# Performance work log

Measured on AMD Instinct MI355X. Metric: run time of the kernel, lower is better.

## Reference

```python
import jax, jax.numpy as jnp
import numpy as np

ALPHA = 0.01  # ELU slope from init kwargs


def setup_inputs() -> dict:
    key = jax.random.key(0)
    k1, k2, k3, k4, k5 = jax.random.split(key, 5)
    B, L, D_IN, D_ATT = 8, 2048, 256, 128
    context = jax.random.normal(k1, (B, L, D_IN), dtype=jnp.float32)
    query = jax.random.normal(k2, (B, L, D_IN), dtype=jnp.float32)
    query_mask = jax.random.randint(k3, (B, L), 0, 2, dtype=jnp.int32)
    # Linear(in_size, attention_size, bias=False) weights (stored as [in, out])
    W_in = jax.random.normal(k4, (D_IN, D_ATT), dtype=jnp.float32) * 0.05
    W_mem = jax.random.normal(k5, (D_IN, D_ATT), dtype=jnp.float32) * 0.05
    return {"context": context, "query": query, "W_in": W_in,
            "W_mem": W_mem, "query_mask": query_mask}


def reference(context, query, W_in, W_mem, query_mask):
    # VariationalDropout is identity at inference; Linear -> ELU(alpha=0.01)
    inp = jax.nn.elu(jnp.einsum('bld,df->blf', context, W_in), ALPHA)   # [B, Lc, Datt]
    mem = jax.nn.elu(jnp.einsum('bld,df->blf', query, W_mem), ALPHA)    # [B, Lq, Datt]
    scale = inp.shape[-1] ** 0.5
    logits = jnp.einsum('bcf,bqf->bcq', inp, mem) / scale               # [B, Lc, Lq]
    big = jnp.finfo(logits.dtype).max
    # mask_diag=True: kill diagonal (self) positions
    Lq = logits.shape[-1]
    eye = jnp.eye(Lq, dtype=bool)
    logits = jnp.where(eye[None, :, :], -big, logits)
    # masked_softmax over the query axis using query_mask [B, Lq]
    valid = (query_mask > 0)[:, None, :]                                # [B, 1, Lq]
    logits = jnp.where(valid, logits, -big)
    score = jax.nn.softmax(logits, axis=-1)                             # [B, Lc, Lq]
    return jnp.einsum('bcq,bqd->bcd', score, query)                     # [B, Lc, D_in]
```

## Files before the change

kernel.cpp:

```cpp
#include <hip/hip_runtime.h>
#include <math.h>

typedef short v4s __attribute__((ext_vector_type(4)));
typedef short v8s __attribute__((ext_vector_type(8)));
typedef float v4f __attribute__((ext_vector_type(4)));

#define L2E 1.4426950408889634f
#define INV_SCALE 0.08838834764831845f
#define SCL2 (INV_SCALE * L2E)

static __device__ __forceinline__ short f2bf(float x) {
    union { float f; unsigned u; } c; c.f = x;
    unsigned u = c.u;
    unsigned r = (u + 0x7fffu + ((u >> 16) & 1u)) >> 16;
    return (short)r;
}

typedef __attribute__((address_space(3))) void lds_vt;
typedef __attribute__((address_space(1))) const void gl_vt;
static __device__ __forceinline__ void gload_lds16(const void* g, void* l) {
    __builtin_amdgcn_global_load_lds((gl_vt*)g, (lds_vt*)l, 16, 0, 0);
}

__global__ __launch_bounds__(256) void k_pre(const float* __restrict__ ctx,
                                             const float* __restrict__ qry,
                                             const float* __restrict__ Win,
                                             const float* __restrict__ Wmem,
                                             const int* __restrict__ qmask,
                                             short* __restrict__ Qa,
                                             short* __restrict__ Ka,
                                             short* __restrict__ VaT,
                                             float* __restrict__ maskadd) {
    __shared__ __align__(16) char sbuf[64 * 264 * 2];
    int x = blockIdx.x;
    int tid = threadIdx.x;
    if (x < 1024) {
        short* WtS = (short*)sbuf;
        int msel = x & 255, isel = (x >> 8) & 1, nh = (x >> 9) & 1;
        const float* X = isel ? qry : ctx;
        const float* W = isel ? Wmem : Win;
        short* Y = isel ? Ka : Qa;
#pragma unroll 8
        for (int i = 0; i < 64; ++i) {
            int id = i * 256 + tid;
            int k = id >> 6, fp = id & 63;
            WtS[fp * 264 + k] = f2bf(W[k * 128 + nh * 64 + fp]);
        }
        __syncthreads();

        int w = tid >> 6, lane = tid & 63;
        int ln = lane & 15, qd = lane >> 4;
        int m0 = msel * 64 + w * 16;
        v4f zero = {0.f, 0.f, 0.f, 0.f};
        v4f o[4];
#pragma unroll
        for (int i = 0; i < 4; ++i) o[i] = zero;
#pragma unroll
        for (int kk = 0; kk < 8; ++kk) {
            const float* xp = X + (size_t)(m0 + ln) * 256 + kk * 32 + qd * 8;
            float4 x0 = *(const float4*)xp;
            float4 x1 = *(const float4*)(xp + 4);
            v8s a;
            a[0] = f2bf(x0.x); a[1] = f2bf(x0.y); a[2] = f2bf(x0.z); a[3] = f2bf(x0.w);
            a[4] = f2bf(x1.x); a[5] = f2bf(x1.y); a[6] = f2bf(x1.z); a[7] = f2bf(x1.w);
#pragma unroll
            for (int nt = 0; nt < 4; ++nt) {
                v8s bfr = *(const v8s*)(WtS + (nt * 16 + ln) * 264 + kk * 32 + qd * 8);
                o[nt] = __builtin_amdgcn_mfma_f32_16x16x32_bf16(a, bfr, o[nt], 0, 0, 0);
            }
        }
#pragma unroll
        for (int nt = 0; nt < 4; ++nt) {
#pragma unroll
            for (int r = 0; r < 4; ++r) {
                float v = o[nt][r];
                v = v > 0.f ? v : 0.01f * (__expf(v) - 1.f);
                Y[(size_t)(m0 + qd * 4 + r) * 128 + (nh * 4 + nt) * 16 + ln] = f2bf(v);
            }
        }
    } else {
        float (*tile)[65] = (float(*)[65])sbuf;
        int t = x - 1024;
        int q0 = (t & 31) * 64, d0 = ((t >> 5) & 3) * 64, b = t >> 7;
        int c = tid & 63;
        int r4 = tid >> 6;
#pragma unroll
        for (int i = 0; i < 16; ++i) {
            int r = r4 + i * 4;
            tile[r][c] = qry[(size_t)(b * 2048 + q0 + r) * 256 + d0 + c];
        }
        __syncthreads();
        int g = c >> 3, j = c & 7;
#pragma unroll
        for (int i = 0; i < 16; ++i) {
            int d = r4 + i * 4;
            int cs = ((g ^ (d & 7)) << 3) | j;
            VaT[(size_t)(b * 256 + d0 + d) * 2048 + q0 + cs] = f2bf(tile[c][d]);
        }
        if (d0 == 0 && tid < 64) {
            int qq = b * 2048 + q0 + tid;
            maskadd[qq] = (qmask[qq] > 0) ? 0.f : -__builtin_inff();
        }
    }
}

__global__ __launch_bounds__(256, 2) void k_attn(const short* __restrict__ Qa,
                                                 const short* __restrict__ Ka,
                                                 const short* __restrict__ VaT,
                                                 const float* __restrict__ maskadd,
                                                 float* __restrict__ out) {
    __shared__ __align__(16) short VaS[2][256 * 64];
    __shared__ __align__(16) short PSb[2][32 * 64];

    const int STEPS = 32;
    int blk = blockIdx.x;
    int b = blk & 7;
    int c0 = (blk >> 3) * 32;

    int tid = threadIdx.x;
    int w = tid >> 6, lane = tid & 63, ln = lane & 15, qd = lane >> 4;

    const short* qbase = Qa + (size_t)(b * 2048) * 128;
    const short* kbase = Ka + (size_t)(b * 2048 + w * 16 + ln) * 128 + qd * 8;
    const short* vbase = VaT + (size_t)(b * 256) * 2048;
    const float* mbase = maskadd + b * 2048 + w * 16 + qd * 4;

    v8s qf[2][4];
#pragma unroll
    for (int ct = 0; ct < 2; ++ct) {
        const short* qp = qbase + (size_t)(c0 + ct * 16 + ln) * 128 + qd * 8;
#pragma unroll
        for (int kk = 0; kk < 4; ++kk) qf[ct][kk] = *(const v8s*)(qp + kk * 32);
    }

    v4f zero = {0.f, 0.f, 0.f, 0.f};
    v4f o[2][4];
#pragma unroll
    for (int i = 0; i < 2; ++i)
#pragma unroll
        for (int j = 0; j < 4; ++j) o[i][j] = zero;
    float lacc[2] = {0.f, 0.f};

    auto stageV = [&](int q0s, int buf) {
        short* base = &VaS[buf][0] + w * 4096;
#pragma unroll
        for (int j = 0; j < 8; ++j) {
            int U = (w * 8 + j) * 64 + lane;
            int d = U >> 3, cc = U & 7;
            gload_lds16(vbase + (size_t)d * 2048 + q0s + cc * 8,
                        base + j * 512);
        }
    };

    stageV(0, 0);
    v8s kfA[4], kfB[4];
    float4 mkA, mkB;
#pragma unroll
    for (int kk = 0; kk < 4; ++kk) kfA[kk] = *(const v8s*)(kbase + kk * 32);
    mkA = *(const float4*)(mbase);

#define ATT_STEP(IT, KFC, MKC, KFN, MKN) do {                                  \
    int q0 = (IT) * 64;                                                        \
    int pb = (IT) & 1;                                                         \
    int itn = ((IT) + 1) & (STEPS - 1);                                        \
    stageV(itn * 64, pb ^ 1);                                                  \
    {                                                                          \
        const short* kp = kbase + (size_t)itn * 8192;                          \
        _Pragma("unroll")                                                      \
        for (int kk = 0; kk < 4; ++kk) KFN[kk] = *(const v8s*)(kp + kk * 32);  \
        MKN = *(const float4*)(mbase + itn * 64);                              \
    }                                                                          \
      \
    asm volatile("s_waitcnt vmcnt(13)" ::: "memory");                          \
    short* PScur = &PSb[pb][0];                                                \
    int kvb = q0 + w * 16 + qd * 4;                                            \
    _Pragma("unroll")                                                          \
    for (int ct = 0; ct < 2; ++ct) {                                           \
        v4f s = zero;                                                          \
        _Pragma("unroll")                                                      \
        for (int kk = 0; kk < 4; ++kk)                                         \
            s = __builtin_amdgcn_mfma_f32_16x16x32_bf16(KFC[kk], qf[ct][kk],   \
                                                        s, 0, 0, 0);           \
        int cg = c0 + ct * 16 + ln;                                            \
        v4s pw;                                                                \
        float ls = 0.f;                                                        \
        _Pragma("unroll")                                                      \
        for (int r = 0; r < 4; ++r) {                                          \
            float v = s[r] * SCL2 + (&MKC.x)[r];                               \
            if (kvb + r == cg) v = -__builtin_inff();                          \
            float p = exp2f(v);                                                \
            ls += p;                                                           \
            pw[r] = f2bf(p);                                                   \
        }                                                                      \
        lacc[ct] += ls;                                                        \
        int hs = ((w * 2 + (qd >> 1)) ^ (ln & 7));                             \
        *(v4s*)(PScur + (ct * 16 + ln) * 64 + hs * 8 + (qd & 1) * 4) = pw;     \
    }                                                                          \
    asm volatile("s_waitcnt lgkmcnt(0)" ::: "memory");                         \
    __builtin_amdgcn_s_barrier();                                              \
    asm volatile("" ::: "memory");                                             \
    const short* vs = &VaS[pb][0];                                             \
    __builtin_amdgcn_s_setprio(1);                                             \
    _Pragma("unroll")                                                          \
    for (int kk2 = 0; kk2 < 2; ++kk2) {                                        \
        v8s pf[2], vf[4];                                                      \
        _Pragma("unroll")                                                      \
        for (int ct = 0; ct < 2; ++ct)                                         \
            pf[ct] = *(const v8s*)(PScur + (ct * 16 + ln) * 64 +               \
                                   (((kk2 * 4 + qd) ^ (ln & 7)) << 3));        \
        _Pragma("unroll")                                                      \
        for (int dt = 0; dt < 4; ++dt) {                                       \
            int d = w * 64 + dt * 16 + ln;                                     \
            vf[dt] = *(const v8s*)(vs + d * 64 +                               \
                                   (((kk2 * 4 + qd) ^ (ln & 7)) << 3));        \
        }                                                                      \
        _Pragma("unroll")                                                      \
        for (int ct = 0; ct < 2; ++ct)                                         \
            _Pragma("unroll")                                                  \
            for (int dt = 0; dt < 4; ++dt)                                     \
                o[ct][dt] = __builtin_amdgcn_mfma_f32_16x16x32_bf16(           \
                    pf[ct], vf[dt], o[ct][dt], 0, 0, 0);                       \
    }                                                                          \
    __builtin_amdgcn_s_setprio(0);                                             \
} while (0)

#pragma unroll 1
    for (int it2 = 0; it2 < STEPS; it2 += 2) {
        ATT_STEP(it2, kfA, mkA, kfB, mkB);
        ATT_STEP(it2 + 1, kfB, mkB, kfA, mkA);
    }
#undef ATT_STEP

    __syncthreads();
    float* lS = (float*)&PSb[0][0];
#pragma unroll
    for (int ct = 0; ct < 2; ++ct) {
        float v = lacc[ct];
        v += __shfl_xor(v, 16);
        v += __shfl_xor(v, 32);
        if (qd == 0) lS[w * 32 + ct * 16 + ln] = v;
    }
    __syncthreads();

#pragma unroll
    for (int ct = 0; ct < 2; ++ct) {
        float4 l0 = *(const float4*)(lS + 0 * 32 + ct * 16 + qd * 4);
        float4 l1 = *(const float4*)(lS + 1 * 32 + ct * 16 + qd * 4);
        float4 l2 = *(const float4*)(lS + 2 * 32 + ct * 16 + qd * 4);
        float4 l3 = *(const float4*)(lS + 3 * 32 + ct * 16 + qd * 4);
        int rowg = b * 2048 + c0 + ct * 16 + qd * 4;
#pragma unroll
        for (int r = 0; r < 4; ++r) {
            float lv = (&l0.x)[r] + (&l1.x)[r] + (&l2.x)[r] + (&l3.x)[r];
            float inv = 1.f / lv;
#pragma unroll
            for (int dt = 0; dt < 4; ++dt)
                out[(size_t)(rowg + r) * 256 + w * 64 + dt * 16 + ln] =
                    o[ct][dt][r] * inv;
        }
    }
}

extern "C" void kernel_launch(void* const* d_in, const int* in_sizes, int n_in,
                              void* d_out, int out_size, void* d_ws, size_t ws_size,
                              hipStream_t stream) {
    const float* ctx  = (const float*)d_in[0];
    const float* qry  = (const float*)d_in[1];
    const float* win  = (const float*)d_in[2];
    const float* wmem = (const float*)d_in[3];
    const int* qmask  = (const int*)d_in[4];
    float* out = (float*)d_out;

    char* ws = (char*)d_ws;
    short* Qa      = (short*)(ws);
    short* Ka      = (short*)(ws + (4u << 20));
    short* VaT     = (short*)(ws + (8u << 20));
    float* maskadd = (float*)(ws + (16u << 20));

    k_pre<<<dim3(2048), 256, 0, stream>>>(ctx, qry, win, wmem, qmask,
                                          Qa, Ka, VaT, maskadd);
    k_attn<<<dim3(512), 256, 0, stream>>>(Qa, Ka, VaT, maskadd, out);
}
```

Before: 152.9 us.

## Enlarge attention query tile, split KV across two blocks, merge partials via atomics

The attention kernel now handles 64 query rows per block instead of 32, so each K/V tile is reused over more rows. To keep the grid at 512 blocks, the KV range is split in two. Each block writes unnormalized partial outputs and row sums to a workspace, and the second block to finish (found via an atomic counter) combines both halves. V staging goes from double-buffered to single-buffered to fit the larger P buffer, and the projection prepass now computes all 128 output columns per block in two K halves. This adds fp32 partial traffic and a serialized merge step, and the single V buffer reduces overlap between loads and compute.

```diff
diff --git a/kernel.cpp b/kernel.cpp
--- a/kernel.cpp
+++ b/kernel.cpp
@@ -30,57 +30,63 @@
                                              short* __restrict__ Qa,
                                              short* __restrict__ Ka,
                                              short* __restrict__ VaT,
-                                             float* __restrict__ maskadd) {
-    __shared__ __align__(16) char sbuf[64 * 264 * 2];
+                                             float* __restrict__ maskadd,
+                                             int* __restrict__ flags) {
+    __shared__ __align__(16) char sbuf[128 * 132 * 2];
     int x = blockIdx.x;
     int tid = threadIdx.x;
-    if (x < 1024) {
+    if (x < 512) {
         short* WtS = (short*)sbuf;
-        int msel = x & 255, isel = (x >> 8) & 1, nh = (x >> 9) & 1;
+        int msel = x & 255, isel = x >> 8;
         const float* X = isel ? qry : ctx;
         const float* W = isel ? Wmem : Win;
         short* Y = isel ? Ka : Qa;
-#pragma unroll 8
-        for (int i = 0; i < 64; ++i) {
-            int id = i * 256 + tid;
-            int k = id >> 6, fp = id & 63;
-            WtS[fp * 264 + k] = f2bf(W[k * 128 + nh * 64 + fp]);
-        }
-        __syncthreads();
 
         int w = tid >> 6, lane = tid & 63;
         int ln = lane & 15, qd = lane >> 4;
         int m0 = msel * 64 + w * 16;
         v4f zero = {0.f, 0.f, 0.f, 0.f};
-        v4f o[4];
-#pragma unroll
-        for (int i = 0; i < 4; ++i) o[i] = zero;
-#pragma unroll
-        for (int kk = 0; kk < 8; ++kk) {
-            const float* xp = X + (size_t)(m0 + ln) * 256 + kk * 32 + qd * 8;
-            float4 x0 = *(const float4*)xp;
-            float4 x1 = *(const float4*)(xp + 4);
-            v8s a;
-            a[0] = f2bf(x0.x); a[1] = f2bf(x0.y); a[2] = f2bf(x0.z); a[3] = f2bf(x0.w);
-            a[4] = f2bf(x1.x); a[5] = f2bf(x1.y); a[6] = f2bf(x1.z); a[7] = f2bf(x1.w);
-#pragma unroll
-            for (int nt = 0; nt < 4; ++nt) {
-                v8s bfr = *(const v8s*)(WtS + (nt * 16 + ln) * 264 + kk * 32 + qd * 8);
-                o[nt] = __builtin_amdgcn_mfma_f32_16x16x32_bf16(a, bfr, o[nt], 0, 0, 0);
-            }
-        }
-#pragma unroll
-        for (int nt = 0; nt < 4; ++nt) {
+        v4f o[8];
+#pragma unroll
+        for (int i = 0; i < 8; ++i) o[i] = zero;
+
+#pragma unroll 1
+        for (int kh = 0; kh < 2; ++kh) {
+            if (kh) __syncthreads();
+#pragma unroll 8
+            for (int i = 0; i < 64; ++i) {
+                int id = i * 256 + tid;
+                int k = id >> 7, fp = id & 127;
+                WtS[fp * 132 + k] = f2bf(W[(kh * 128 + k) * 128 + fp]);
+            }
+            __syncthreads();
+#pragma unroll
+            for (int kk = 0; kk < 4; ++kk) {
+                const float* xp = X + (size_t)(m0 + ln) * 256 + kh * 128 + kk * 32 + qd * 8;
+                float4 x0 = *(const float4*)xp;
+                float4 x1 = *(const float4*)(xp + 4);
+                v8s a;
+                a[0] = f2bf(x0.x); a[1] = f2bf(x0.y); a[2] = f2bf(x0.z); a[3] = f2bf(x0.w);
+                a[4] = f2bf(x1.x); a[5] = f2bf(x1.y); a[6] = f2bf(x1.z); a[7] = f2bf(x1.w);
+#pragma unroll
+                for (int nt = 0; nt < 8; ++nt) {
+                    v8s bfr = *(const v8s*)(WtS + (nt * 16 + ln) * 132 + kk * 32 + qd * 8);
+                    o[nt] = __builtin_amdgcn_mfma_f32_16x16x32_bf16(a, bfr, o[nt], 0, 0, 0);
+                }
+            }
+        }
+#pragma unroll
+        for (int nt = 0; nt < 8; ++nt) {
 #pragma unroll
             for (int r = 0; r < 4; ++r) {
                 float v = o[nt][r];
                 v = v > 0.f ? v : 0.01f * (__expf(v) - 1.f);
-                Y[(size_t)(m0 + qd * 4 + r) * 128 + (nh * 4 + nt) * 16 + ln] = f2bf(v);
+                Y[(size_t)(m0 + qd * 4 + r) * 128 + nt * 16 + ln] = f2bf(v);
             }
         }
     } else {
         float (*tile)[65] = (float(*)[65])sbuf;
-        int t = x - 1024;
+        int t = x - 512;
         int q0 = (t & 31) * 64, d0 = ((t >> 5) & 3) * 64, b = t >> 7;
         int c = tid & 63;
         int r4 = tid >> 6;
@@ -101,48 +107,57 @@
             int qq = b * 2048 + q0 + tid;
             maskadd[qq] = (qmask[qq] > 0) ? 0.f : -__builtin_inff();
         }
-    }
-}
-
+        if (t == 0) flags[tid] = 0;
+    }
+}
+
+template<int NSPLIT, bool DIRECT>
 __global__ __launch_bounds__(256, 2) void k_attn(const short* __restrict__ Qa,
                                                  const short* __restrict__ Ka,
                                                  const short* __restrict__ VaT,
                                                  const float* __restrict__ maskadd,
+                                                 float* __restrict__ Opart,
+                                                 float* __restrict__ lpart,
+                                                 int* __restrict__ flags,
                                                  float* __restrict__ out) {
-    __shared__ __align__(16) short VaS[2][256 * 64];
-    __shared__ __align__(16) short PSb[2][32 * 64];
-
-    const int STEPS = 32;
+    __shared__ __align__(16) short VaS[256 * 64];
+    __shared__ __align__(16) short PSb[2][64 * 64];
+    __shared__ int who;
+
+    const int STEPS = 32 / NSPLIT;
     int blk = blockIdx.x;
     int b = blk & 7;
-    int c0 = (blk >> 3) * 32;
+    int t = blk >> 3;
+    int c0 = (t & 31) * 64;
+    int sp = t >> 5;
+    int kv0 = sp * (2048 / NSPLIT);
 
     int tid = threadIdx.x;
     int w = tid >> 6, lane = tid & 63, ln = lane & 15, qd = lane >> 4;
 
     const short* qbase = Qa + (size_t)(b * 2048) * 128;
-    const short* kbase = Ka + (size_t)(b * 2048 + w * 16 + ln) * 128 + qd * 8;
+    const short* kbase = Ka + (size_t)(b * 2048 + kv0 + w * 16 + ln) * 128 + qd * 8;
     const short* vbase = VaT + (size_t)(b * 256) * 2048;
-    const float* mbase = maskadd + b * 2048 + w * 16 + qd * 4;
-
-    v8s qf[2][4];
-#pragma unroll
-    for (int ct = 0; ct < 2; ++ct) {
+    const float* mbase = maskadd + b * 2048 + kv0 + w * 16 + qd * 4;
+
+    v8s qf[4][4];
+#pragma unroll
+    for (int ct = 0; ct < 4; ++ct) {
         const short* qp = qbase + (size_t)(c0 + ct * 16 + ln) * 128 + qd * 8;
 #pragma unroll
         for (int kk = 0; kk < 4; ++kk) qf[ct][kk] = *(const v8s*)(qp + kk * 32);
     }
 
     v4f zero = {0.f, 0.f, 0.f, 0.f};
-    v4f o[2][4];
-#pragma unroll
-    for (int i = 0; i < 2; ++i)
+    v4f o[4][4];
+#pragma unroll
+    for (int i = 0; i < 4; ++i)
 #pragma unroll
         for (int j = 0; j < 4; ++j) o[i][j] = zero;
-    float lacc[2] = {0.f, 0.f};
-
-    auto stageV = [&](int q0s, int buf) {
-        short* base = &VaS[buf][0] + w * 4096;
+    float lacc[4] = {0.f, 0.f, 0.f, 0.f};
+
+    auto stageV = [&](int q0s) {
+        short* base = &VaS[0] + w * 4096;
 #pragma unroll
         for (int j = 0; j < 8; ++j) {
             int U = (w * 8 + j) * 64 + lane;
@@ -152,30 +167,27 @@
         }
     };
 
-    stageV(0, 0);
     v8s kfA[4], kfB[4];
     float4 mkA, mkB;
 #pragma unroll
     for (int kk = 0; kk < 4; ++kk) kfA[kk] = *(const v8s*)(kbase + kk * 32);
     mkA = *(const float4*)(mbase);
+    stageV(kv0);
 
 #define ATT_STEP(IT, KFC, MKC, KFN, MKN) do {                                  \
-    int q0 = (IT) * 64;                                                        \
+    int q0 = kv0 + (IT) * 64;                                                  \
     int pb = (IT) & 1;                                                         \
     int itn = ((IT) + 1) & (STEPS - 1);                                        \
-    stageV(itn * 64, pb ^ 1);                                                  \
-    {                                                                          \
+    {              \
         const short* kp = kbase + (size_t)itn * 8192;                          \
         _Pragma("unroll")                                                      \
         for (int kk = 0; kk < 4; ++kk) KFN[kk] = *(const v8s*)(kp + kk * 32);  \
         MKN = *(const float4*)(mbase + itn * 64);                              \
     }                                                                          \
-      \
-    asm volatile("s_waitcnt vmcnt(13)" ::: "memory");                          \
     short* PScur = &PSb[pb][0];                                                \
     int kvb = q0 + w * 16 + qd * 4;                                            \
     _Pragma("unroll")                                                          \
-    for (int ct = 0; ct < 2; ++ct) {                                           \
+    for (int ct = 0; ct < 4; ++ct) {                                           \
         v4f s = zero;                                                          \
         _Pragma("unroll")                                                      \
         for (int kk = 0; kk < 4; ++kk)                                         \
@@ -198,14 +210,15 @@
     }                                                                          \
     asm volatile("s_waitcnt lgkmcnt(0)" ::: "memory");                         \
     __builtin_amdgcn_s_barrier();                                              \
-    asm volatile("" ::: "memory");                                             \
-    const short* vs = &VaS[pb][0];                                             \
+        \
+    asm volatile("s_waitcnt vmcnt(5)" ::: "memory");                           \
+    const short* vs = &VaS[0];                                                 \
     __builtin_amdgcn_s_setprio(1);                                             \
     _Pragma("unroll")                                                          \
     for (int kk2 = 0; kk2 < 2; ++kk2) {                                        \
-        v8s pf[2], vf[4];                                                      \
-        _Pragma("unroll")                                                      \
-        for (int ct = 0; ct < 2; ++ct)                                         \
+        v8s pf[4], vf[4];                                                      \
+        _Pragma("unroll")                                                      \
+        for (int ct = 0; ct < 4; ++ct)                                         \
             pf[ct] = *(const v8s*)(PScur + (ct * 16 + ln) * 64 +               \
                                    (((kk2 * 4 + qd) ^ (ln & 7)) << 3));        \
         _Pragma("unroll")                                                      \
@@ -215,13 +228,16 @@
                                    (((kk2 * 4 + qd) ^ (ln & 7)) << 3));        \
         }                                                                      \
         _Pragma("unroll")                                                      \
-        for (int ct = 0; ct < 2; ++ct)                                         \
+        for (int ct = 0; ct < 4; ++ct)                                         \
             _Pragma("unroll")                                                  \
             for (int dt = 0; dt < 4; ++dt)                                     \
                 o[ct][dt] = __builtin_amdgcn_mfma_f32_16x16x32_bf16(           \
                     pf[ct], vf[dt], o[ct][dt], 0, 0, 0);                       \
     }                                                                          \
     __builtin_amdgcn_s_setprio(0);                                             \
+             \
+    asm volatile("s_waitcnt lgkmcnt(0)" ::: "memory");                         \
+    stageV(kv0 + itn * 64);                                                    \
 } while (0)
 
 #pragma unroll 1
@@ -234,29 +250,78 @@
     __syncthreads();
     float* lS = (float*)&PSb[0][0];
 #pragma unroll
-    for (int ct = 0; ct < 2; ++ct) {
+    for (int ct = 0; ct < 4; ++ct) {
         float v = lacc[ct];
         v += __shfl_xor(v, 16);
         v += __shfl_xor(v, 32);
-        if (qd == 0) lS[w * 32 + ct * 16 + ln] = v;
+        if (qd == 0) lS[w * 64 + ct * 16 + ln] = v;
     }
     __syncthreads();
 
-#pragma unroll
-    for (int ct = 0; ct < 2; ++ct) {
-        float4 l0 = *(const float4*)(lS + 0 * 32 + ct * 16 + qd * 4);
-        float4 l1 = *(const float4*)(lS + 1 * 32 + ct * 16 + qd * 4);
-        float4 l2 = *(const float4*)(lS + 2 * 32 + ct * 16 + qd * 4);
-        float4 l3 = *(const float4*)(lS + 3 * 32 + ct * 16 + qd * 4);
-        int rowg = b * 2048 + c0 + ct * 16 + qd * 4;
-#pragma unroll
-        for (int r = 0; r < 4; ++r) {
-            float lv = (&l0.x)[r] + (&l1.x)[r] + (&l2.x)[r] + (&l3.x)[r];
-            float inv = 1.f / lv;
-#pragma unroll
-            for (int dt = 0; dt < 4; ++dt)
-                out[(size_t)(rowg + r) * 256 + w * 64 + dt * 16 + ln] =
-                    o[ct][dt][r] * inv;
+    float flv[4][4];
+#pragma unroll
+    for (int ct = 0; ct < 4; ++ct) {
+        float4 l0 = *(const float4*)(lS + 0 * 64 + ct * 16 + qd * 4);
+        float4 l1 = *(const float4*)(lS + 1 * 64 + ct * 16 + qd * 4);
+        float4 l2 = *(const float4*)(lS + 2 * 64 + ct * 16 + qd * 4);
+        float4 l3 = *(const float4*)(lS + 3 * 64 + ct * 16 + qd * 4);
+#pragma unroll
+        for (int r = 0; r < 4; ++r)
+            flv[ct][r] = (&l0.x)[r] + (&l1.x)[r] + (&l2.x)[r] + (&l3.x)[r];
+    }
+
+    if (DIRECT) {
+#pragma unroll
+        for (int ct = 0; ct < 4; ++ct) {
+            int rowg = b * 2048 + c0 + ct * 16 + qd * 4;
+#pragma unroll
+            for (int r = 0; r < 4; ++r) {
+                float inv = 1.f / flv[ct][r];
+#pragma unroll
+                for (int dt = 0; dt < 4; ++dt)
+                    out[(size_t)(rowg + r) * 256 + w * 64 + dt * 16 + ln] =
+                        o[ct][dt][r] * inv;
+            }
+        }
+    } else {
+        float* op = Opart + (size_t)sp * (16384 * 256);
+#pragma unroll
+        for (int ct = 0; ct < 4; ++ct) {
+            int rowg = b * 2048 + c0 + ct * 16 + qd * 4;
+#pragma unroll
+            for (int r = 0; r < 4; ++r)
+#pragma unroll
+                for (int dt = 0; dt < 4; ++dt)
+                    op[(size_t)(rowg + r) * 256 + w * 64 + dt * 16 + ln] = o[ct][dt][r];
+            if (ln == 0)
+                *(float4*)(lpart + sp * 16384 + rowg) =
+                    make_float4(flv[ct][0], flv[ct][1], flv[ct][2], flv[ct][3]);
+        }
+        __threadfence();
+        if (tid == 0) {
+            int pair = b * 32 + (t & 31);
+            who = __hip_atomic_fetch_add(&flags[pair], 1, __ATOMIC_ACQ_REL,
+                                         __HIP_MEMORY_SCOPE_AGENT);
+        }
+        __syncthreads();
+        if (who == 0) return;
+
+        int osp = sp ^ 1;
+        const float* oo = Opart + (size_t)osp * (16384 * 256);
+        const float* ol = lpart + osp * 16384;
+#pragma unroll
+        for (int ct = 0; ct < 4; ++ct) {
+            int rowg = b * 2048 + c0 + ct * 16 + qd * 4;
+#pragma unroll
+            for (int r = 0; r < 4; ++r) {
+                float inv = 1.f / (flv[ct][r] + ol[rowg + r]);
+#pragma unroll
+                for (int dt = 0; dt < 4; ++dt) {
+                    int col = w * 64 + dt * 16 + ln;
+                    float sum = o[ct][dt][r] + oo[(size_t)(rowg + r) * 256 + col];
+                    out[(size_t)(rowg + r) * 256 + col] = sum * inv;
+                }
+            }
         }
     }
 }
@@ -276,8 +341,19 @@
     short* Ka      = (short*)(ws + (4u << 20));
     short* VaT     = (short*)(ws + (8u << 20));
     float* maskadd = (float*)(ws + (16u << 20));
-
-    k_pre<<<dim3(2048), 256, 0, stream>>>(ctx, qry, win, wmem, qmask,
-                                          Qa, Ka, VaT, maskadd);
-    k_attn<<<dim3(512), 256, 0, stream>>>(Qa, Ka, VaT, maskadd, out);
-}
+    int*   flags   = (int*)(ws + (16u << 20) + 65536);
+    float* lpart   = (float*)(ws + (16u << 20) + 131072);
+    float* Opart   = (float*)(ws + (18u << 20));
+
+    k_pre<<<dim3(1536), 256, 0, stream>>>(ctx, qry, win, wmem, qmask,
+                                          Qa, Ka, VaT, maskadd, flags);
+
+    const size_t base = 18u << 20, part = 16u << 20;
+    if (ws_size >= base + 2 * part) {
+        k_attn<2, false><<<dim3(512), 256, 0, stream>>>(Qa, Ka, VaT, maskadd,
+                                                        Opart, lpart, flags, out);
+    } else {
+        k_attn<1, true><<<dim3(256), 256, 0, stream>>>(Qa, Ka, VaT, maskadd,
+                                                       Opart, lpart, flags, out);
+    }
+}
```

New measurement: 229.5 us. 50.1% more time.
